# Kernel tuning notes

Measured on AMD Instinct MI355X. Metric: run time of the kernel, lower is better.

The kernel has to match this reference:

```python
import jax, jax.numpy as jnp
import numpy as np

DIM = 512
HEADS = 8
D_HEAD = DIM // HEADS
SCALE = D_HEAD ** -0.5


def setup_inputs() -> dict:
    key = jax.random.key(0)
    k_x, k_qkv, k_ow, k_ob = jax.random.split(key, 4)
    x = jax.random.normal(k_x, (2, 4096, DIM), dtype=jnp.float32)
    # nn.Linear stores weight as [out, in]; y = x @ W.T
    w_qkv = jax.random.normal(k_qkv, (3 * DIM, DIM), dtype=jnp.float32) * (DIM ** -0.5)
    w_out = jax.random.normal(k_ow, (DIM, DIM), dtype=jnp.float32) * (DIM ** -0.5)
    b_out = jax.random.normal(k_ob, (DIM,), dtype=jnp.float32) * 0.01
    return {"x": x, "w_qkv": w_qkv, "w_out": w_out, "b_out": b_out}


def reference(x, w_qkv, w_out, b_out):
    B, S, _ = x.shape
    qkv = jnp.einsum('bsd,ed->bse', x, w_qkv)            # [B,S,3*DIM]
    q, k, v = jnp.split(qkv, 3, axis=-1)
    # [B,S,DIM] -> [B,H,S,Dh]
    def split_heads(t):
        return t.reshape(B, S, HEADS, D_HEAD).transpose(0, 2, 1, 3)
    q, k, v = split_heads(q), split_heads(k), split_heads(v)
    dots = jnp.einsum('bhqd,bhkd->bhqk', q, k) * SCALE   # [B,H,S,S]
    attn = jax.nn.softmax(dots, axis=-1)
    out = jnp.einsum('bhqk,bhkd->bhqd', attn, v)         # [B,H,S,Dh]
    out = out.transpose(0, 2, 1, 3).reshape(B, S, DIM)
    return jnp.einsum('bsd,ed->bse', out, w_out) + b_out
```

## Files before the change

### kernel.cpp

```cpp
#include <hip/hip_runtime.h>
#include <math.h>

#define BATCH 2
#define SEQ   4096
#define DIM   512
#define HEADS 8
#define DH    64

typedef _Float16 f16;
typedef __attribute__((ext_vector_type(8)))  _Float16 f16x8;
typedef __attribute__((ext_vector_type(4)))  _Float16 f16x4;
typedef __attribute__((ext_vector_type(2)))  __fp16   h16x2;
typedef __attribute__((ext_vector_type(4)))  float f32x4;
typedef __attribute__((ext_vector_type(16))) float f32x16;

#if __has_builtin(__builtin_amdgcn_exp2f)
#define EXP2F(x) __builtin_amdgcn_exp2f(x)
#else
#define EXP2F(x) exp2f(x)
#endif

__device__ __forceinline__ void gload_lds16(const void* g, void* l) {
  __builtin_amdgcn_global_load_lds(
      (const __attribute__((address_space(1))) unsigned int*)g,
      (__attribute__((address_space(3))) unsigned int*)l, 16, 0, 0);
}

__device__ __forceinline__ unsigned pk2(float a, float b) {
    h16x2 h = __builtin_amdgcn_cvt_pkrtz(a, b);
    union { h16x2 h; unsigned u; } c; c.h = h; return c.u;
}
__device__ __forceinline__ void pl32swap(unsigned &a, unsigned &b) {
    asm volatile("v_permlane32_swap_b32 %0, %1" : "+v"(a), "+v"(b));
}
__device__ __forceinline__ float dot2acc(unsigned w, float acc) {
#if __has_builtin(__builtin_amdgcn_fdot2)
    union { unsigned u; h16x2 h; } c; c.u = w;
    h16x2 one = {(__fp16)1.0f, (__fp16)1.0f};
    return __builtin_amdgcn_fdot2(c.h, one, acc, false);
#else
    union { unsigned u; __fp16 h[2]; } c; c.u = w;
    return acc + (float)c.h[0] + (float)c.h[1];
#endif
}

__global__ __launch_bounds__(256) void prep_kernel(
    const float* __restrict__ x, const float* __restrict__ wqkv,
    const float* __restrict__ wout,
    f16* __restrict__ xh, f16* __restrict__ wqh, f16* __restrict__ woh)
{
    int i4 = (blockIdx.x * 256 + threadIdx.x) * 4;
    const float* src; f16* dh; int idx;
    if (i4 < 4194304)      { src = x;    dh = xh;  idx = i4; }
    else if (i4 < 4980736) { src = wqkv; dh = wqh; idx = i4 - 4194304; }
    else                   { src = wout; dh = woh; idx = i4 - 4980736; }
    float4 v = *(const float4*)(src + idx);
    f16x4 h;
    h[0] = (f16)v.x; h[1] = (f16)v.y; h[2] = (f16)v.z; h[3] = (f16)v.w;
    *(f16x4*)(dh + idx) = h;
}

__global__ __launch_bounds__(256) void qkv_mfma_kernel(
    const f16* __restrict__ xh_, const f16* __restrict__ wh,
    f16* __restrict__ qh, f16* __restrict__ kh, f16* __restrict__ vth)
{
    __shared__ __align__(16) char smem[32768];
    const int t = threadIdx.x, lane = t & 63, wave = t >> 6;
    const int l15 = lane & 15, l4 = lane >> 4;
    const int m0 = blockIdx.x * 64;
    const int n0 = blockIdx.y * 64;
    const int which = blockIdx.y >> 3;
    const int h     = blockIdx.y & 7;

    const int r0 = t >> 3,         c0 = (t & 7) ^ (r0 & 7);
    const int r1 = (t + 256) >> 3, c1 = ((t + 256) & 7) ^ (r1 & 7);

#define STAGEQ(k0, dbase)                                                     \
    do {                                                                      \
        gload_lds16(xh_ + (size_t)(m0 + r0) * DIM + (k0) + c0 * 8,            \
                    smem + (dbase) + t * 16);                                 \
        gload_lds16(xh_ + (size_t)(m0 + r1) * DIM + (k0) + c1 * 8,            \
                    smem + (dbase) + (t + 256) * 16);                         \
        gload_lds16(wh + (size_t)(n0 + r0) * DIM + (k0) + c0 * 8,             \
                    smem + (dbase) + 8192 + t * 16);                          \
        gload_lds16(wh + (size_t)(n0 + r1) * DIM + (k0) + c1 * 8,             \
                    smem + (dbase) + 8192 + (t + 256) * 16);                  \
    } while (0)

    f32x4 acc[4];
#pragma unroll
    for (int nb = 0; nb < 4; ++nb) acc[nb] = (f32x4){0.f, 0.f, 0.f, 0.f};

    STAGEQ(0, 0);
    __syncthreads();

    for (int ks = 0; ks < 8; ++ks) {
        const int cur = ks & 1;
        if (ks < 7) STAGEQ((ks + 1) * 64, (cur ^ 1) * 16384);
        const char* bX = smem + cur * 16384;
        const char* bW = bX + 8192;

        f16x8 ah[2];
        const int arow = wave * 16 + l15;
#pragma unroll
        for (int kb = 0; kb < 2; ++kb) {
            int ac = (l4 + 4 * kb) ^ (arow & 7);
            ah[kb] = *(const f16x8*)(bX + arow * 128 + ac * 16);
        }
#pragma unroll
        for (int nb = 0; nb < 4; ++nb) {
            const int brow = nb * 16 + l15;
#pragma unroll
            for (int kb = 0; kb < 2; ++kb) {
                int bc = (l4 + 4 * kb) ^ (brow & 7);
                f16x8 b_h = *(const f16x8*)(bW + brow * 128 + bc * 16);
                acc[nb] = __builtin_amdgcn_mfma_f32_16x16x32_f16(ah[kb], b_h, acc[nb], 0, 0, 0);
            }
        }
        __syncthreads();
    }

    if (which < 2) {
        const float scale = (which == 0) ? 0.125f * 1.44269504f : 1.0f;
        f16* dst = (which == 0) ? qh : kh;
#pragma unroll
        for (int nb = 0; nb < 4; ++nb) {
            int d = nb * 16 + l15;
#pragma unroll
            for (int r = 0; r < 4; ++r) {
                int m  = m0 + wave * 16 + l4 * 4 + r;
                int b_ = m >> 12, s = m & (SEQ - 1);
                dst[((size_t)((b_ * HEADS + h) * SEQ + s)) * DH + d] =
                    (f16)(acc[nb][r] * scale);
            }
        }
    } else {
        float* T = (float*)smem;
#pragma unroll
        for (int nb = 0; nb < 4; ++nb)
#pragma unroll
            for (int r = 0; r < 4; ++r) {
                int lm = wave * 16 + l4 * 4 + r;
                T[lm * 65 + nb * 16 + l15] = acc[nb][r];
            }
        __syncthreads();
        const int dr  = t >> 2;
        const int sc0 = (t & 3) * 16;
        const int b_  = m0 >> 12;
        const int sbase = (m0 & (SEQ - 1)) + sc0;
        size_t obase = ((size_t)((b_ * HEADS + h) * DH + dr)) * SEQ + sbase;
#pragma unroll
        for (int g = 0; g < 2; ++g) {
            f16x8 hv;
#pragma unroll
            for (int j = 0; j < 8; ++j)
                hv[j] = (f16)T[(sc0 + g * 8 + j) * 65 + dr];
            *(f16x8*)(vth + obase + g * 8) = hv;
        }
    }
#undef STAGEQ
}

__global__ __launch_bounds__(512, 4) void attn_mfma_kernel(
    const f16* __restrict__ qh_,
    const f16* __restrict__ kh_, const f16* __restrict__ vth_,
    f16* __restrict__ o_h)
{
    __shared__ __align__(16) char smem[65536];
    const int t = threadIdx.x, lane = t & 63, wave = t >> 6;
    const int q31 = lane & 31, h5 = lane >> 5;
    const int grp = wave >> 2, w4 = wave & 3;
    const int bid  = blockIdx.x;
    const int flat = (bid & 7) * 64 + (bid >> 3);
    const int qt = flat & 31, bh = flat >> 5;
    const int q0 = qt * 128;

    const f16* kgb = kh_  + (size_t)bh * SEQ * DH;
    const f16* vgb = vth_ + (size_t)bh * DH * SEQ;

    const int srow = t >> 3, sgc = (t & 7) ^ (srow & 7);

#define STAGE(kvn, dbase)                                                     \
    do {                                                                      \
        gload_lds16(kgb + (size_t)((kvn) + srow) * DH + sgc * 8,              \
                    smem + (dbase) + t * 16);                                 \
        gload_lds16(vgb + (size_t)srow * SEQ + (kvn) + sgc * 8,               \
                    smem + (dbase) + 8192 + t * 16);                          \
        gload_lds16(kgb + (size_t)((kvn) + 64 + srow) * DH + sgc * 8,         \
                    smem + (dbase) + 16384 + t * 16);                         \
        gload_lds16(vgb + (size_t)srow * SEQ + (kvn) + 64 + sgc * 8,          \
                    smem + (dbase) + 24576 + t * 16);                         \
    } while (0)

    f16x8 qfh[4];
    {
        const int qrow = q0 + w4 * 32 + q31;
        size_t base = ((size_t)bh * SEQ + qrow) * DH + h5 * 8;
#pragma unroll
        for (int ks = 0; ks < 4; ++ks)
            qfh[ks] = *(const f16x8*)(qh_ + base + ks * 16);
    }

    f32x16 o_acc[2];
#pragma unroll
    for (int dt = 0; dt < 2; ++dt)
#pragma unroll
        for (int r = 0; r < 16; ++r) o_acc[dt][r] = 0.f;
    float run_l = 0.f;

    STAGE(0, 0);
    __syncthreads();

    const int NT = SEQ / 128;
    for (int s = 0; s < NT; ++s) {
        const int cur = s & 1;
        if (s + 1 < NT) STAGE((s + 1) * 128, (cur ^ 1) * 32768);
        const char* bK = smem + cur * 32768 + grp * 16384;
        const char* bV = bK + 8192;

        f32x16 sacc[2];
        __builtin_amdgcn_s_setprio(1);
#pragma unroll
        for (int jb = 0; jb < 2; ++jb) {
            f32x16 a;
#pragma unroll
            for (int r = 0; r < 16; ++r) a[r] = 0.f;
            const int krow = 32 * jb + q31;
#pragma unroll
            for (int ks = 0; ks < 4; ++ks) {
                int slot = (h5 + 2 * ks) ^ (krow & 7);
                f16x8 kf = *(const f16x8*)(bK + krow * 128 + slot * 16);
                a = __builtin_amdgcn_mfma_f32_32x32x16_f16(kf, qfh[ks], a, 0, 0, 0);
            }
            sacc[jb] = a;
        }
        __builtin_amdgcn_s_setprio(0);

        float ls0 = 0.f, ls1 = 0.f, ls2 = 0.f, ls3 = 0.f;
        unsigned pw[2][8];
#pragma unroll
        for (int jb = 0; jb < 2; ++jb)
#pragma unroll
            for (int k = 0; k < 8; ++k) {
                float p0 = EXP2F(sacc[jb][2 * k]);
                float p1 = EXP2F(sacc[jb][2 * k + 1]);
                pw[jb][k] = pk2(p0, p1);
                switch (k & 3) {
                    case 0: ls0 = dot2acc(pw[jb][k], ls0); break;
                    case 1: ls1 = dot2acc(pw[jb][k], ls1); break;
                    case 2: ls2 = dot2acc(pw[jb][k], ls2); break;
                    default: ls3 = dot2acc(pw[jb][k], ls3); break;
                }
            }
        float ls = (ls0 + ls1) + (ls2 + ls3);
        ls += __shfl_xor(ls, 32);
        run_l += ls;

        __builtin_amdgcn_s_setprio(1);
#pragma unroll
        for (int ks = 0; ks < 4; ++ks) {
            const int jb = ks >> 1, c = (ks & 1) * 4;
            unsigned y0a = pw[jb][c + 0];
            unsigned y0b = pw[jb][c + 1];
            unsigned y1a = pw[jb][c + 2];
            unsigned y1b = pw[jb][c + 3];
            pl32swap(y0a, y1a);
            pl32swap(y0b, y1b);
            union { f16x8 v; unsigned u[4]; } bb;
            bb.u[0] = y0a; bb.u[1] = y0b; bb.u[2] = y1a; bb.u[3] = y1b;
#pragma unroll
            for (int dt = 0; dt < 2; ++dt) {
                const int vrow = 32 * dt + q31;
                int vslot = (h5 + 2 * ks) ^ (vrow & 7);
                f16x8 vb = *(const f16x8*)(bV + vrow * 128 + vslot * 16);
                o_acc[dt] = __builtin_amdgcn_mfma_f32_32x32x16_f16(vb, bb.v, o_acc[dt], 0, 0, 0);
            }
        }
        __builtin_amdgcn_s_setprio(0);

        __syncthreads();
    }

    if (grp == 1) {
        float* mb = (float*)(smem + w4 * 9216 + lane * 144);
#pragma unroll
        for (int dt = 0; dt < 2; ++dt)
#pragma unroll
            for (int rr = 0; rr < 4; ++rr) {
                float4 v4 = {o_acc[dt][rr*4+0], o_acc[dt][rr*4+1],
                             o_acc[dt][rr*4+2], o_acc[dt][rr*4+3]};
                *(float4*)(mb + dt * 16 + rr * 4) = v4;
            }
        mb[32] = run_l;
    }
    __syncthreads();
    if (grp == 0) {
        const float* mb = (const float*)(smem + wave * 9216 + lane * 144);
        float invl = 1.0f / (run_l + mb[32]);

        char* ep = smem + 36864 + wave * 4096;
#pragma unroll
        for (int dt = 0; dt < 2; ++dt)
#pragma unroll
            for (int rr = 0; rr < 4; ++rr) {
                float4 vB = *(const float4*)(mb + dt * 16 + rr * 4);
                f16x4 ov;
                ov[0] = (f16)((o_acc[dt][rr*4+0] + vB.x) * invl);
                ov[1] = (f16)((o_acc[dt][rr*4+1] + vB.y) * invl);
                ov[2] = (f16)((o_acc[dt][rr*4+2] + vB.z) * invl);
                ov[3] = (f16)((o_acc[dt][rr*4+3] + vB.w) * invl);
                int g = rr + 4 * dt;
                *(f16x4*)(ep + q31 * 128 + ((g ^ (q31 & 7)) * 16) + 8 * h5) = ov;
            }
        const int b_ = bh >> 3, hh = bh & 7;
#pragma unroll
        for (int itc = 0; itc < 4; ++itc) {
            int ch = lane + itc * 64;
            int row = ch >> 3, g = ch & 7;
            f16x8 v = *(const f16x8*)(ep + row * 128 + ((g ^ (row & 7)) * 16));
            int s = q0 + wave * 32 + row;
            *(f16x8*)(o_h + ((size_t)(b_ * SEQ + s)) * DIM + hh * DH + g * 8) = v;
        }
    }
#undef STAGE
}

__global__ __launch_bounds__(256) void oproj_mfma_kernel(
    const f16* __restrict__ oh, const f16* __restrict__ wh,
    const float* __restrict__ bias, float* __restrict__ out)
{
    __shared__ __align__(16) char smem[32768];
    const int t = threadIdx.x, lane = t & 63, wave = t >> 6;
    const int l15 = lane & 15, l4 = lane >> 4;
    const int m0 = blockIdx.x * 64;
    const int n0 = blockIdx.y * 64;

    const int r0 = t >> 3,         c0 = (t & 7) ^ (r0 & 7);
    const int r1 = (t + 256) >> 3, c1 = ((t + 256) & 7) ^ (r1 & 7);

#define STAGEO(k0, dbase)                                                     \
    do {                                                                      \
        gload_lds16(oh + (size_t)(m0 + r0) * DIM + (k0) + c0 * 8,             \
                    smem + (dbase) + t * 16);                                 \
        gload_lds16(oh + (size_t)(m0 + r1) * DIM + (k0) + c1 * 8,             \
                    smem + (dbase) + (t + 256) * 16);                         \
        gload_lds16(wh + (size_t)(n0 + r0) * DIM + (k0) + c0 * 8,             \
                    smem + (dbase) + 8192 + t * 16);                          \
        gload_lds16(wh + (size_t)(n0 + r1) * DIM + (k0) + c1 * 8,             \
                    smem + (dbase) + 8192 + (t + 256) * 16);                  \
    } while (0)

    f32x4 acc[4];
#pragma unroll
    for (int nb = 0; nb < 4; ++nb) acc[nb] = (f32x4){0.f, 0.f, 0.f, 0.f};

    STAGEO(0, 0);
    __syncthreads();

    for (int ks = 0; ks < 8; ++ks) {
        const int cur = ks & 1;
        if (ks < 7) STAGEO((ks + 1) * 64, (cur ^ 1) * 16384);
        const char* bO = smem + cur * 16384;
        const char* bW = bO + 8192;

        f16x8 ah[2];
        const int arow = wave * 16 + l15;
#pragma unroll
        for (int kb = 0; kb < 2; ++kb) {
            int ac = (l4 + 4 * kb) ^ (arow & 7);
            ah[kb] = *(const f16x8*)(bO + arow * 128 + ac * 16);
        }
#pragma unroll
        for (int nb = 0; nb < 4; ++nb) {
            const int brow = nb * 16 + l15;
#pragma unroll
            for (int kb = 0; kb < 2; ++kb) {
                int bc = (l4 + 4 * kb) ^ (brow & 7);
                f16x8 b_h = *(const f16x8*)(bW + brow * 128 + bc * 16);
                acc[nb] = __builtin_amdgcn_mfma_f32_16x16x32_f16(ah[kb], b_h, acc[nb], 0, 0, 0);
            }
        }
        __syncthreads();
    }

#pragma unroll
    for (int nb = 0; nb < 4; ++nb) {
        int n = n0 + nb * 16 + l15;
        float bz = bias[n];
#pragma unroll
        for (int r = 0; r < 4; ++r) {
            int m = m0 + wave * 16 + l4 * 4 + r;
            out[(size_t)m * DIM + n] = acc[nb][r] + bz;
        }
    }
#undef STAGEO
}

extern "C" void kernel_launch(void* const* d_in, const int* in_sizes, int n_in,
                              void* d_out, int out_size, void* d_ws, size_t ws_size,
                              hipStream_t stream) {
    const float* x     = (const float*)d_in[0];
    const float* w_qkv = (const float*)d_in[1];
    const float* w_out = (const float*)d_in[2];
    const float* b_out = (const float*)d_in[3];
    float* out = (float*)d_out;

    const size_t per = (size_t)BATCH * HEADS * SEQ * DH;
    f16* base = (f16*)d_ws;
    f16* xh  = base;
    f16* wqh = xh + per;
    f16* woh = wqh + 786432;
    f16* qh  = woh + 262144;
    f16* kh  = qh + per;
    f16* vth = kh + per;
    f16* o_h = vth + per;

    prep_kernel<<<5120, 256, 0, stream>>>(x, w_qkv, w_out, xh, wqh, woh);
    qkv_mfma_kernel<<<dim3(128, 24), 256, 0, stream>>>(xh, wqh, qh, kh, vth);
    attn_mfma_kernel<<<512, 512, 0, stream>>>(qh, kh, vth, o_h);
    oproj_mfma_kernel<<<dim3(128, 8), 256, 0, stream>>>(o_h, woh, b_out, out);
}
```

Before: 117.1 us.

## Load K fragments directly into registers, stage only V through LDS

K tiles are no longer staged through shared memory. Each lane now loads its K MFMA fragments straight from global memory into registers, prefetching the next tile right after the QK MFMAs. LDS traffic and footprint drop, with only V double-buffered. In exchange the kernel uses more VGPRs (8 f16x8 fragments), which may hurt occupancy at launch bounds (512,4). It also relies on global-load latency being hidden behind the softmax and PV work.

```diff
diff --git a/kernel.cpp b/kernel.cpp
--- a/kernel.cpp
+++ b/kernel.cpp
@@ -166,7 +166,7 @@
     const f16* __restrict__ kh_, const f16* __restrict__ vth_,
     f16* __restrict__ o_h)
 {
-    __shared__ __align__(16) char smem[65536];
+    __shared__ __align__(16) char smem[53248];
     const int t = threadIdx.x, lane = t & 63, wave = t >> 6;
     const int q31 = lane & 31, h5 = lane >> 5;
     const int grp = wave >> 2, w4 = wave & 3;
@@ -182,14 +182,23 @@
 
 #define STAGE(kvn, dbase)                                                     \
     do {                                                                      \
-        gload_lds16(kgb + (size_t)((kvn) + srow) * DH + sgc * 8,              \
+        gload_lds16(vgb + (size_t)srow * SEQ + (kvn) + sgc * 8,               \
                     smem + (dbase) + t * 16);                                 \
-        gload_lds16(vgb + (size_t)srow * SEQ + (kvn) + sgc * 8,               \
+        gload_lds16(vgb + (size_t)srow * SEQ + (kvn) + 64 + sgc * 8,          \
                     smem + (dbase) + 8192 + t * 16);                          \
-        gload_lds16(kgb + (size_t)((kvn) + 64 + srow) * DH + sgc * 8,         \
-                    smem + (dbase) + 16384 + t * 16);                         \
-        gload_lds16(vgb + (size_t)srow * SEQ + (kvn) + 64 + sgc * 8,          \
-                    smem + (dbase) + 24576 + t * 16);                         \
+    } while (0)
+
+#define LOADK(kvb)                                                            \
+    do {                                                                      \
+        const f16* kp_ = kgb + (size_t)((kvb) + q31) * DH + h5 * 8;           \
+        kf[0] = *(const f16x8*)(kp_ + 0);                                     \
+        kf[1] = *(const f16x8*)(kp_ + 16);                                    \
+        kf[2] = *(const f16x8*)(kp_ + 32);                                    \
+        kf[3] = *(const f16x8*)(kp_ + 48);                                    \
+        kf[4] = *(const f16x8*)(kp_ + 32 * DH + 0);                           \
+        kf[5] = *(const f16x8*)(kp_ + 32 * DH + 16);                          \
+        kf[6] = *(const f16x8*)(kp_ + 32 * DH + 32);                          \
+        kf[7] = *(const f16x8*)(kp_ + 32 * DH + 48);                          \
     } while (0)
 
     f16x8 qfh[4];
@@ -208,15 +217,16 @@
         for (int r = 0; r < 16; ++r) o_acc[dt][r] = 0.f;
     float run_l = 0.f;
 
+    f16x8 kf[8];
+    LOADK(grp * 64);
     STAGE(0, 0);
     __syncthreads();
 
     const int NT = SEQ / 128;
     for (int s = 0; s < NT; ++s) {
         const int cur = s & 1;
-        if (s + 1 < NT) STAGE((s + 1) * 128, (cur ^ 1) * 32768);
-        const char* bK = smem + cur * 32768 + grp * 16384;
-        const char* bV = bK + 8192;
+        if (s + 1 < NT) STAGE((s + 1) * 128, (cur ^ 1) * 16384);
+        const char* bV = smem + cur * 16384 + grp * 8192;
 
         f32x16 sacc[2];
         __builtin_amdgcn_s_setprio(1);
@@ -225,16 +235,14 @@
             f32x16 a;
 #pragma unroll
             for (int r = 0; r < 16; ++r) a[r] = 0.f;
-            const int krow = 32 * jb + q31;
-#pragma unroll
-            for (int ks = 0; ks < 4; ++ks) {
-                int slot = (h5 + 2 * ks) ^ (krow & 7);
-                f16x8 kf = *(const f16x8*)(bK + krow * 128 + slot * 16);
-                a = __builtin_amdgcn_mfma_f32_32x32x16_f16(kf, qfh[ks], a, 0, 0, 0);
-            }
+#pragma unroll
+            for (int ks = 0; ks < 4; ++ks)
+                a = __builtin_amdgcn_mfma_f32_32x32x16_f16(kf[jb * 4 + ks], qfh[ks], a, 0, 0, 0);
             sacc[jb] = a;
         }
         __builtin_amdgcn_s_setprio(0);
+
+        if (s + 1 < NT) LOADK((s + 1) * 128 + grp * 64);
 
         float ls0 = 0.f, ls1 = 0.f, ls2 = 0.f, ls3 = 0.f;
         unsigned pw[2][8];
@@ -323,6 +331,7 @@
         }
     }
 #undef STAGE
+#undef LOADK
 }
 
 __global__ __launch_bounds__(256) void oproj_mfma_kernel(
```

Result: slower. 173.6 us (+48.3%).

## Store K and V in MFMA-fragment-packed tiles to simplify staging and LDS reads

Applied to the files above, without the earlier changes.

The projection kernel now writes K and V directly in a per-64-row tile layout that matches the MFMA operand fragment order. The attention kernel can then stage each tile with contiguous loads and read fragments as lane-linear 16-byte LDS accesses, with no XOR swizzle address math. This also removes the LDS transpose and extra barrier used for V in the projection epilogue. In exchange, the K stores in the projection are scattered 2-byte writes, and the layout is tightly coupled to the fragment indexing, so any mismatch corrupts results.

```diff
diff --git a/kernel.cpp b/kernel.cpp
--- a/kernel.cpp
+++ b/kernel.cpp
@@ -120,9 +120,8 @@
         __syncthreads();
     }
 
-    if (which < 2) {
-        const float scale = (which == 0) ? 0.125f * 1.44269504f : 1.0f;
-        f16* dst = (which == 0) ? qh : kh;
+    if (which == 0) {
+        const float qscale = 0.125f * 1.44269504f;
 #pragma unroll
         for (int nb = 0; nb < 4; ++nb) {
             int d = nb * 16 + l15;
@@ -130,32 +129,41 @@
             for (int r = 0; r < 4; ++r) {
                 int m  = m0 + wave * 16 + l4 * 4 + r;
                 int b_ = m >> 12, s = m & (SEQ - 1);
-                dst[((size_t)((b_ * HEADS + h) * SEQ + s)) * DH + d] =
-                    (f16)(acc[nb][r] * scale);
+                qh[((size_t)((b_ * HEADS + h) * SEQ + s)) * DH + d] =
+                    (f16)(acc[nb][r] * qscale);
+            }
+        }
+    } else if (which == 1) {
+        const int tile = (m0 & (SEQ - 1)) >> 6;
+        const int b_   = m0 >> 12;
+        const int bh   = b_ * HEADS + h;
+        f16* kb = kh + (size_t)bh * SEQ * DH + (size_t)tile * 4096;
+        const int jb  = wave >> 1;
+        const int h5w = l15 >> 3, jj = l15 & 7;
+#pragma unroll
+        for (int nb = 0; nb < 4; ++nb) {
+#pragma unroll
+            for (int r = 0; r < 4; ++r) {
+                int q31 = (wave & 1) * 16 + l4 * 4 + r;
+                kb[(jb * 4 + nb) * 512 + (h5w * 32 + q31) * 8 + jj] =
+                    (f16)acc[nb][r];
             }
         }
     } else {
-        float* T = (float*)smem;
-#pragma unroll
-        for (int nb = 0; nb < 4; ++nb)
-#pragma unroll
-            for (int r = 0; r < 4; ++r) {
-                int lm = wave * 16 + l4 * 4 + r;
-                T[lm * 65 + nb * 16 + l15] = acc[nb][r];
-            }
-        __syncthreads();
-        const int dr  = t >> 2;
-        const int sc0 = (t & 3) * 16;
-        const int b_  = m0 >> 12;
-        const int sbase = (m0 & (SEQ - 1)) + sc0;
-        size_t obase = ((size_t)((b_ * HEADS + h) * DH + dr)) * SEQ + sbase;
-#pragma unroll
-        for (int g = 0; g < 2; ++g) {
-            f16x8 hv;
-#pragma unroll
-            for (int j = 0; j < 8; ++j)
-                hv[j] = (f16)T[(sc0 + g * 8 + j) * 65 + dr];
-            *(f16x8*)(vth + obase + g * 8) = hv;
+        const int tile = (m0 & (SEQ - 1)) >> 6;
+        const int b_   = m0 >> 12;
+        const int bh   = b_ * HEADS + h;
+        f16* vb = vth + (size_t)bh * SEQ * DH + (size_t)tile * 4096;
+        const int h5p = l4 >> 1;
+        const int j0  = (l4 * 4) & 7;
+#pragma unroll
+        for (int nb = 0; nb < 4; ++nb) {
+            f16x4 v;
+#pragma unroll
+            for (int r = 0; r < 4; ++r) v[r] = (f16)acc[nb][r];
+            int off = ((nb >> 1) * 4 + wave) * 512 +
+                      (h5p * 32 + (nb & 1) * 16 + l15) * 8 + j0;
+            *(f16x4*)(vb + off) = v;
         }
     }
 #undef STAGEQ
@@ -176,19 +184,17 @@
     const int q0 = qt * 128;
 
     const f16* kgb = kh_  + (size_t)bh * SEQ * DH;
-    const f16* vgb = vth_ + (size_t)bh * DH * SEQ;
-
-    const int srow = t >> 3, sgc = (t & 7) ^ (srow & 7);
-
-#define STAGE(kvn, dbase)                                                     \
+    const f16* vgb = vth_ + (size_t)bh * SEQ * DH;
+
+#define STAGE(s2, dbase)                                                      \
     do {                                                                      \
-        gload_lds16(kgb + (size_t)((kvn) + srow) * DH + sgc * 8,              \
+        gload_lds16(kgb + (size_t)(2 * (s2)) * 4096 + t * 8,                  \
                     smem + (dbase) + t * 16);                                 \
-        gload_lds16(vgb + (size_t)srow * SEQ + (kvn) + sgc * 8,               \
+        gload_lds16(vgb + (size_t)(2 * (s2)) * 4096 + t * 8,                  \
                     smem + (dbase) + 8192 + t * 16);                          \
-        gload_lds16(kgb + (size_t)((kvn) + 64 + srow) * DH + sgc * 8,         \
+        gload_lds16(kgb + (size_t)(2 * (s2) + 1) * 4096 + t * 8,              \
                     smem + (dbase) + 16384 + t * 16);                         \
-        gload_lds16(vgb + (size_t)srow * SEQ + (kvn) + 64 + sgc * 8,          \
+        gload_lds16(vgb + (size_t)(2 * (s2) + 1) * 4096 + t * 8,              \
                     smem + (dbase) + 24576 + t * 16);                         \
     } while (0)
 
@@ -214,7 +220,7 @@
     const int NT = SEQ / 128;
     for (int s = 0; s < NT; ++s) {
         const int cur = s & 1;
-        if (s + 1 < NT) STAGE((s + 1) * 128, (cur ^ 1) * 32768);
+        if (s + 1 < NT) STAGE(s + 1, (cur ^ 1) * 32768);
         const char* bK = smem + cur * 32768 + grp * 16384;
         const char* bV = bK + 8192;
 
@@ -225,11 +231,9 @@
             f32x16 a;
 #pragma unroll
             for (int r = 0; r < 16; ++r) a[r] = 0.f;
-            const int krow = 32 * jb + q31;
 #pragma unroll
             for (int ks = 0; ks < 4; ++ks) {
-                int slot = (h5 + 2 * ks) ^ (krow & 7);
-                f16x8 kf = *(const f16x8*)(bK + krow * 128 + slot * 16);
+                f16x8 kf = *(const f16x8*)(bK + (jb * 4 + ks) * 1024 + lane * 16);
                 a = __builtin_amdgcn_mfma_f32_32x32x16_f16(kf, qfh[ks], a, 0, 0, 0);
             }
             sacc[jb] = a;
@@ -270,9 +274,7 @@
             bb.u[0] = y0a; bb.u[1] = y0b; bb.u[2] = y1a; bb.u[3] = y1b;
 #pragma unroll
             for (int dt = 0; dt < 2; ++dt) {
-                const int vrow = 32 * dt + q31;
-                int vslot = (h5 + 2 * ks) ^ (vrow & 7);
-                f16x8 vb = *(const f16x8*)(bV + vrow * 128 + vslot * 16);
+                f16x8 vb = *(const f16x8*)(bV + (dt * 4 + ks) * 1024 + lane * 16);
                 o_acc[dt] = __builtin_amdgcn_mfma_f32_32x32x16_f16(vb, bb.v, o_acc[dt], 0, 0, 0);
             }
         }
```

New measurement: 114.5 us. -2.2%, faster.
